# Kernel tuning notes

Hardware: AMD Instinct MI355X
Metric: run time of the kernel (lower is better)

The kernel has to match this reference:

```python
import jax, jax.numpy as jnp
import numpy as np

EMB = 64
HID = 1024
SEQ = 9
BATCH = 4096


def setup_inputs() -> dict:
    key = jax.random.key(0)
    ks = jax.random.split(key, 10)
    s = lambda *sh: 1.0 / np.sqrt(sh[-1])
    return {
        "observed": jax.random.normal(ks[0], (SEQ, BATCH, 2), dtype=jnp.float32),
        "W_emb": jax.random.normal(ks[1], (EMB, 2), dtype=jnp.float32) * s(2),
        "b_emb": jnp.zeros((EMB,), dtype=jnp.float32),
        "W_ih": jax.random.normal(ks[2], (4 * HID, EMB), dtype=jnp.float32) * s(EMB),
        "b_ih": jnp.zeros((4 * HID,), dtype=jnp.float32),
        "W_hh": jax.random.normal(ks[3], (4 * HID, HID), dtype=jnp.float32) * s(HID),
        "b_hh": jnp.zeros((4 * HID,), dtype=jnp.float32),
        "W_out": jax.random.normal(ks[4], (5, HID), dtype=jnp.float32) * s(HID),
        "b_out": jnp.zeros((5,), dtype=jnp.float32),
        "n_predict": 12,
    }


def _cell(x, h, c, W_ih, b_ih, W_hh, b_hh):
    # torch.nn.LSTMCell gate math, gate order i, f, g, o
    gates = x @ W_ih.T + b_ih + h @ W_hh.T + b_hh  # [B, 4H]
    i, f, g, o = jnp.split(gates, 4, axis=-1)
    c_new = jax.nn.sigmoid(f) * c + jax.nn.sigmoid(i) * jnp.tanh(g)
    h_new = jax.nn.sigmoid(o) * jnp.tanh(c_new)
    return h_new, c_new


def reference(observed, W_emb, b_emb, W_ih, b_ih, W_hh, b_hh, W_out, b_out, n_predict):
    B = observed.shape[1]
    H = W_hh.shape[1]
    h0 = jnp.zeros((B, H), dtype=observed.dtype)
    c0 = jnp.zeros((B, H), dtype=observed.dtype)

    diffs = observed[1:] - observed[:-1]  # [SEQ-1, B, 2]

    def obs_step(carry, d):
        h, c = carry
        emb = jax.nn.relu(d @ W_emb.T + b_emb)  # [B, EMB]
        h, c = _cell(emb, h, c, W_ih, b_ih, W_hh, b_hh)
        normal = h @ W_out.T + b_out  # [B, 5]
        return (h, c), normal

    (h, c), normals_obs = jax.lax.scan(obs_step, (h0, c0), diffs)
    new_vel = normals_obs[-1][:, :2]

    def pred_step(carry, _):
        h, c, nv = carry
        emb = jax.nn.relu(jax.lax.stop_gradient(nv) @ W_emb.T + b_emb)
        h, c = _cell(emb, h, c, W_ih, b_ih, W_hh, b_hh)
        normal = h @ W_out.T + b_out
        return (h, c, normal[:, :2]), normal

    (_, _, _), normals_pred = jax.lax.scan(
        pred_step, (h, c, new_vel), None, length=n_predict - 1)

    # training-mode output: stacked raw 'normal' params, shape [SEQ-1+n_predict-1, B, 5]
    return jnp.concatenate([normals_obs, normals_pred], axis=0)
```

## Files before the change

kernel.cpp:

```cpp
#include <hip/hip_runtime.h>
#include <stdint.h>
#include <stddef.h>

#define BATCH 4096
#define HID   1024
#define EMB   64
#define NKH   32
#define NSTEP 19
#define NOBS  8
#define WSL   139264

typedef _Float16 f16;
typedef _Float16 half8 __attribute__((ext_vector_type(8)));
typedef float    float4v __attribute__((ext_vector_type(4)));

__device__ __forceinline__ float sigm(float x) { return 1.f / (1.f + __expf(-x)); }
__device__ __forceinline__ float tanh_f(float x) { return 1.f - 2.f / (__expf(2.f * x) + 1.f); }

__global__ void pack_kernel(const float* __restrict__ W_ih, const float* __restrict__ b_ih,
                            const float* __restrict__ W_hh, const float* __restrict__ b_hh,
                            f16* __restrict__ Wsw, float* __restrict__ bc) {
  int gid = blockIdx.x * blockDim.x + threadIdx.x;
  int tt = gid / WSL;
  int rem = gid - tt * WSL;
  int kt = rem >> 12;
  int ni = (rem >> 9) & 7;
  int lane = (rem >> 3) & 63;
  int e = rem & 7;
  int p = tt * 128 + ni * 16 + (lane & 15);
  int g = (p >> 4) & 3;
  int u = (p >> 8) * 64 + ((p >> 6) & 3) * 16 + (p & 15);
  int orig = g * HID + u;
  int k = kt * 32 + ((lane >> 4) << 3) + e;
  float val = (k < EMB) ? W_ih[orig * EMB + k] : W_hh[orig * HID + (k - EMB)];
  Wsw[gid] = (f16)val;
  if (k == 0) bc[p] = b_ih[orig] + b_hh[orig];
}

__global__ __launch_bounds__(256, 3)
void gemm_cell_kernel(const f16* __restrict__ Xp, const f16* __restrict__ Wsw,
                      const float* __restrict__ bc,
                      f16* __restrict__ c_ws, f16* __restrict__ Xn,
                      float* __restrict__ po_ws, const float* __restrict__ W_out,
                      const float* __restrict__ obs_t, const float* __restrict__ outprev,
                      int mode, const float* __restrict__ W_emb,
                      const float* __restrict__ b_emb) {
  __shared__ float pol[64 * 4 * 5];

  const int tid = threadIdx.x;
  const int lane = tid & 63;
  const int wn = tid >> 6;
  const int l15 = lane & 15;
  const int quad = lane >> 4;
  const int sh = wn >> 1, nq = wn & 1;

  const int id = blockIdx.x;
  const int x = id & 7, rr0 = id >> 3;
  const int bn = x * 2 + (rr0 & 1);
  const int bm = rr0 >> 1;
  const int slice = bn * 2 + sh;

  float4v acc[4][4];
#pragma unroll
  for (int mi = 0; mi < 4; ++mi)
#pragma unroll
    for (int ni = 0; ni < 4; ++ni) acc[mi][ni] = (float4v){0.f, 0.f, 0.f, 0.f};

  const f16* aB = Xp + (size_t)(bm * 4) * (NKH * 512) + lane * 8;
  const f16* bB = Wsw + (size_t)slice * WSL + (size_t)2 * 4096 + (nq * 4) * 512 + lane * 8;

  {
    float d0[4], d1[4];
#pragma unroll
    for (int mi = 0; mi < 4; ++mi) {
      const int row = (bm * 4 + mi) * 16 + l15;
      if (mode <= 1) {
        const float* o = obs_t + (size_t)row * 2;
        d0[mi] = o[BATCH * 2] - o[0];
        d1[mi] = o[BATCH * 2 + 1] - o[1];
      } else {
        d0[mi] = outprev[(size_t)row * 5 + 0];
        d1[mi] = outprev[(size_t)row * 5 + 1];
      }
    }
#pragma unroll
    for (int kt = 0; kt < 2; ++kt) {
      float w0[8], w1[8], be[8];
#pragma unroll
      for (int e = 0; e < 8; ++e) {
        const int j = kt * 32 + quad * 8 + e;
        w0[e] = W_emb[2 * j];
        w1[e] = W_emb[2 * j + 1];
        be[e] = b_emb[j];
      }
      half8 bfe[4];
#pragma unroll
      for (int ni = 0; ni < 4; ++ni)
        bfe[ni] = *(const half8*)(Wsw + (size_t)slice * WSL + kt * 4096 + (nq * 4 + ni) * 512 + lane * 8);
#pragma unroll
      for (int mi = 0; mi < 4; ++mi) {
        half8 ae;
#pragma unroll
        for (int e = 0; e < 8; ++e)
          ae[e] = (f16)fmaxf(d0[mi] * w0[e] + d1[mi] * w1[e] + be[e], 0.f);
#pragma unroll
        for (int ni = 0; ni < 4; ++ni)
          acc[mi][ni] = __builtin_amdgcn_mfma_f32_16x16x32_f16(ae, bfe[ni], acc[mi][ni], 0, 0, 0);
      }
    }
  }

  if (mode != 0) {
    half8 afA[4], bfA[4], afB[4], bfB[4];
#define LOADF(af, bf, kh)                                                      \
  do {                                                                         \
    _Pragma("unroll") for (int mi = 0; mi < 4; ++mi)                           \
        af[mi] = *(const half8*)(aB + mi * (NKH * 512) + (kh) * 512);          \
    _Pragma("unroll") for (int ni = 0; ni < 4; ++ni)                           \
        bf[ni] = *(const half8*)(bB + (size_t)(kh) * 4096 + ni * 512);         \
  } while (0)
#define MFMA_ALL(af, bf)                                                       \
  do {                                                                         \
    __builtin_amdgcn_s_setprio(1);                                             \
    _Pragma("unroll") for (int mi = 0; mi < 4; ++mi)                           \
    _Pragma("unroll") for (int ni = 0; ni < 4; ++ni)                           \
        acc[mi][ni] =                                                          \
            __builtin_amdgcn_mfma_f32_16x16x32_f16(af[mi], bf[ni], acc[mi][ni], 0, 0, 0); \
    __builtin_amdgcn_s_setprio(0);                                             \
  } while (0)
    LOADF(afA, bfA, 0);
    for (int i = 0; i < NKH / 2; ++i) {
      const int k1 = 2 * i + 1;
      LOADF(afB, bfB, k1);
      MFMA_ALL(afA, bfA);
      if (k1 + 1 < NKH) LOADF(afA, bfA, k1 + 1);
      MFMA_ALL(afB, bfB);
    }
#undef LOADF
#undef MFMA_ALL
  }

  float bb[4];
#pragma unroll
  for (int ni = 0; ni < 4; ++ni) bb[ni] = bc[bn * 256 + wn * 64 + ni * 16 + l15];
  const int u = bn * 64 + wn * 16 + l15;
  float wo[5];
#pragma unroll
  for (int o = 0; o < 5; ++o) wo[o] = W_out[o * HID + u];

  f16* cbase = c_ws + ((size_t)(bm * 16 + bn) * 256 + tid) * 16;
  half8 cv[2];
  if (mode != 0) {
#pragma unroll
    for (int q = 0; q < 2; ++q) cv[q] = *(const half8*)(cbase + q * 8);
  }

#pragma unroll
  for (int mi = 0; mi < 4; ++mi) {
#pragma unroll
    for (int r = 0; r < 4; ++r) {
      const int rl = mi * 16 + quad * 4 + r;
      const int row = bm * 64 + rl;
      const int ci = mi * 4 + r;
      float gi = acc[mi][0][r] + bb[0];
      float gf = acc[mi][1][r] + bb[1];
      float gg = acc[mi][2][r] + bb[2];
      float go = acc[mi][3][r] + bb[3];
      float co = (mode == 0) ? 0.f : (float)cv[ci >> 3][ci & 7];
      float cn = sigm(gf) * co + sigm(gi) * tanh_f(gg);
      cv[ci >> 3][ci & 7] = (f16)cn;
      float h = sigm(go) * tanh_f(cn);
      Xn[(((size_t)(row >> 4) * NKH + slice) * 64 + (quad * 4 + r) +
          16 * ((wn & 1) * 2 + (l15 >> 3))) * 8 + (l15 & 7)] = (f16)h;
      float pa[5];
#pragma unroll
      for (int o = 0; o < 5; ++o) pa[o] = h * wo[o];
#pragma unroll
      for (int o = 0; o < 5; ++o) {
        pa[o] += __shfl_xor(pa[o], 1, 64);
        pa[o] += __shfl_xor(pa[o], 2, 64);
        pa[o] += __shfl_xor(pa[o], 4, 64);
        pa[o] += __shfl_xor(pa[o], 8, 64);
      }
      if (l15 == 0) {
#pragma unroll
        for (int o = 0; o < 5; ++o) pol[(rl * 4 + wn) * 5 + o] = pa[o];
      }
    }
  }
#pragma unroll
  for (int q = 0; q < 2; ++q) *(half8*)(cbase + q * 8) = cv[q];

  __syncthreads();
  for (int idx = tid; idx < 320; idx += 256) {
    const int rl = idx / 5, o = idx - rl * 5;
    float s = 0.f;
#pragma unroll
    for (int j = 0; j < 4; ++j) s += pol[(rl * 4 + j) * 5 + o];
    po_ws[((size_t)bn * BATCH + bm * 64 + rl) * 5 + o] = s;
  }
}

__global__ __launch_bounds__(256)
void reduce_kernel(const float* __restrict__ po_ws, const float* __restrict__ b_out,
                   float* __restrict__ out_t) {
  const int tid = threadIdx.x;
  const int r0 = blockIdx.x * 32;
  if (tid < 160) {
    const int rowl = tid / 5, o = tid - rowl * 5;
    const int row = r0 + rowl;
    float s = 0.f;
#pragma unroll
    for (int g = 0; g < 16; ++g) s += po_ws[((size_t)g * BATCH + row) * 5 + o];
    out_t[(size_t)row * 5 + o] = s + b_out[o];
  }
}

extern "C" void kernel_launch(void* const* d_in, const int* in_sizes, int n_in,
                              void* d_out, int out_size, void* d_ws, size_t ws_size,
                              hipStream_t stream) {
  const float* observed = (const float*)d_in[0];
  const float* W_emb = (const float*)d_in[1];
  const float* b_emb = (const float*)d_in[2];
  const float* W_ih = (const float*)d_in[3];
  const float* b_ih = (const float*)d_in[4];
  const float* W_hh = (const float*)d_in[5];
  const float* b_hh = (const float*)d_in[6];
  const float* W_out = (const float*)d_in[7];
  const float* b_out = (const float*)d_in[8];
  float* out = (float*)d_out;

  uint8_t* ws = (uint8_t*)d_ws;
  const size_t WSW_BYTES = (size_t)32 * WSL * sizeof(f16);
  const size_t XH_BYTES = (size_t)256 * NKH * 64 * 8 * sizeof(f16);
  f16* Wsw = (f16*)ws;
  float* bc = (float*)(ws + WSW_BYTES);
  f16* X0 = (f16*)(ws + WSW_BYTES + 16384);
  f16* X1 = (f16*)(ws + WSW_BYTES + 16384 + XH_BYTES);
  f16* c_ws = (f16*)(ws + WSW_BYTES + 16384 + 2 * XH_BYTES);
  float* po_ws = (float*)(ws + WSW_BYTES + 16384 + 2 * XH_BYTES + (size_t)BATCH * HID * 2);

  pack_kernel<<<(32 * WSL) / 256, 256, 0, stream>>>(W_ih, b_ih, W_hh, b_hh, Wsw, bc);

  for (int t = 0; t < NSTEP; ++t) {
    f16* Xc = (t & 1) ? X1 : X0;
    f16* Xq = (t & 1) ? X0 : X1;
    const int mode = (t == 0) ? 0 : (t < NOBS ? 1 : 2);
    gemm_cell_kernel<<<1024, 256, 0, stream>>>(
        Xq, Wsw, bc, c_ws, Xc, po_ws, W_out,
        observed + (size_t)t * BATCH * 2, out + (size_t)(t - 1) * BATCH * 5,
        mode, W_emb, b_emb);
    reduce_kernel<<<BATCH / 32, 256, 0, stream>>>(po_ws, b_out, out + (size_t)t * BATCH * 5);
  }
}
```

Measured before the change: 1.135 ms.

## Move output projection out of GEMM epilogue into separate kernel reading h

The W_out projection, with its shuffle reductions, shared-memory partials and per-slice partial-sum buffer, is removed from the LSTM GEMM epilogue. A new out_kernel reads the fp16 h from the swizzled X buffer and computes the 5 outputs per row with one wave per row. The K loop is also rewritten as a fully unrolled double-buffered loop. This trims epilogue work and register pressure in the main kernel. In exchange it re-reads h from memory and computes the projection from fp16-rounded h instead of fp32 h.

```diff
diff --git a/kernel.cpp b/kernel.cpp
--- a/kernel.cpp
+++ b/kernel.cpp
@@ -41,12 +41,9 @@
 void gemm_cell_kernel(const f16* __restrict__ Xp, const f16* __restrict__ Wsw,
                       const float* __restrict__ bc,
                       f16* __restrict__ c_ws, f16* __restrict__ Xn,
-                      float* __restrict__ po_ws, const float* __restrict__ W_out,
                       const float* __restrict__ obs_t, const float* __restrict__ outprev,
                       int mode, const float* __restrict__ W_emb,
                       const float* __restrict__ b_emb) {
-  __shared__ float pol[64 * 4 * 5];
-
   const int tid = threadIdx.x;
   const int lane = tid & 63;
   const int wn = tid >> 6;
@@ -67,7 +64,7 @@
     for (int ni = 0; ni < 4; ++ni) acc[mi][ni] = (float4v){0.f, 0.f, 0.f, 0.f};
 
   const f16* aB = Xp + (size_t)(bm * 4) * (NKH * 512) + lane * 8;
-  const f16* bB = Wsw + (size_t)slice * WSL + (size_t)2 * 4096 + (nq * 4) * 512 + lane * 8;
+  const f16* bB = Wsw + (size_t)slice * WSL + 2 * 4096 + (nq * 4) * 512 + lane * 8;
 
   {
     float d0[4], d1[4];
@@ -111,42 +108,33 @@
   }
 
   if (mode != 0) {
-    half8 afA[4], bfA[4], afB[4], bfB[4];
-#define LOADF(af, bf, kh)                                                      \
+    half8 af[2][4], bf[2][4];
+#define LOADT(buf, kh)                                                         \
   do {                                                                         \
     _Pragma("unroll") for (int mi = 0; mi < 4; ++mi)                           \
-        af[mi] = *(const half8*)(aB + mi * (NKH * 512) + (kh) * 512);          \
+        af[buf][mi] = *(const half8*)(aB + mi * (NKH * 512) + (kh) * 512);     \
     _Pragma("unroll") for (int ni = 0; ni < 4; ++ni)                           \
-        bf[ni] = *(const half8*)(bB + (size_t)(kh) * 4096 + ni * 512);         \
+        bf[buf][ni] = *(const half8*)(bB + (kh) * 4096 + ni * 512);            \
   } while (0)
-#define MFMA_ALL(af, bf)                                                       \
-  do {                                                                         \
-    __builtin_amdgcn_s_setprio(1);                                             \
-    _Pragma("unroll") for (int mi = 0; mi < 4; ++mi)                           \
-    _Pragma("unroll") for (int ni = 0; ni < 4; ++ni)                           \
-        acc[mi][ni] =                                                          \
-            __builtin_amdgcn_mfma_f32_16x16x32_f16(af[mi], bf[ni], acc[mi][ni], 0, 0, 0); \
-    __builtin_amdgcn_s_setprio(0);                                             \
-  } while (0)
-    LOADF(afA, bfA, 0);
-    for (int i = 0; i < NKH / 2; ++i) {
-      const int k1 = 2 * i + 1;
-      LOADF(afB, bfB, k1);
-      MFMA_ALL(afA, bfA);
-      if (k1 + 1 < NKH) LOADF(afA, bfA, k1 + 1);
-      MFMA_ALL(afB, bfB);
-    }
-#undef LOADF
-#undef MFMA_ALL
+    LOADT(0, 0);
+#pragma unroll
+    for (int kh = 0; kh < NKH; ++kh) {
+      if (kh + 1 < NKH) LOADT((kh + 1) & 1, kh + 1);
+      __builtin_amdgcn_s_setprio(1);
+#pragma unroll
+      for (int mi = 0; mi < 4; ++mi)
+#pragma unroll
+        for (int ni = 0; ni < 4; ++ni)
+          acc[mi][ni] = __builtin_amdgcn_mfma_f32_16x16x32_f16(af[kh & 1][mi], bf[kh & 1][ni],
+                                                               acc[mi][ni], 0, 0, 0);
+      __builtin_amdgcn_s_setprio(0);
+    }
+#undef LOADT
   }
 
   float bb[4];
 #pragma unroll
   for (int ni = 0; ni < 4; ++ni) bb[ni] = bc[bn * 256 + wn * 64 + ni * 16 + l15];
-  const int u = bn * 64 + wn * 16 + l15;
-  float wo[5];
-#pragma unroll
-  for (int o = 0; o < 5; ++o) wo[o] = W_out[o * HID + u];
 
   f16* cbase = c_ws + ((size_t)(bm * 16 + bn) * 256 + tid) * 16;
   half8 cv[2];
@@ -159,8 +147,7 @@
   for (int mi = 0; mi < 4; ++mi) {
 #pragma unroll
     for (int r = 0; r < 4; ++r) {
-      const int rl = mi * 16 + quad * 4 + r;
-      const int row = bm * 64 + rl;
+      const int row = bm * 64 + mi * 16 + quad * 4 + r;
       const int ci = mi * 4 + r;
       float gi = acc[mi][0][r] + bb[0];
       float gf = acc[mi][1][r] + bb[1];
@@ -172,47 +159,48 @@
       float h = sigm(go) * tanh_f(cn);
       Xn[(((size_t)(row >> 4) * NKH + slice) * 64 + (quad * 4 + r) +
           16 * ((wn & 1) * 2 + (l15 >> 3))) * 8 + (l15 & 7)] = (f16)h;
-      float pa[5];
-#pragma unroll
-      for (int o = 0; o < 5; ++o) pa[o] = h * wo[o];
-#pragma unroll
-      for (int o = 0; o < 5; ++o) {
-        pa[o] += __shfl_xor(pa[o], 1, 64);
-        pa[o] += __shfl_xor(pa[o], 2, 64);
-        pa[o] += __shfl_xor(pa[o], 4, 64);
-        pa[o] += __shfl_xor(pa[o], 8, 64);
-      }
-      if (l15 == 0) {
-#pragma unroll
-        for (int o = 0; o < 5; ++o) pol[(rl * 4 + wn) * 5 + o] = pa[o];
-      }
     }
   }
 #pragma unroll
   for (int q = 0; q < 2; ++q) *(half8*)(cbase + q * 8) = cv[q];
-
-  __syncthreads();
-  for (int idx = tid; idx < 320; idx += 256) {
-    const int rl = idx / 5, o = idx - rl * 5;
-    float s = 0.f;
-#pragma unroll
-    for (int j = 0; j < 4; ++j) s += pol[(rl * 4 + j) * 5 + o];
-    po_ws[((size_t)bn * BATCH + bm * 64 + rl) * 5 + o] = s;
-  }
 }
 
 __global__ __launch_bounds__(256)
-void reduce_kernel(const float* __restrict__ po_ws, const float* __restrict__ b_out,
-                   float* __restrict__ out_t) {
+void out_kernel(const f16* __restrict__ Xh, const float* __restrict__ W_out,
+                const float* __restrict__ b_out, float* __restrict__ out_t) {
   const int tid = threadIdx.x;
-  const int r0 = blockIdx.x * 32;
-  if (tid < 160) {
-    const int rowl = tid / 5, o = tid - rowl * 5;
-    const int row = r0 + rowl;
-    float s = 0.f;
-#pragma unroll
-    for (int g = 0; g < 16; ++g) s += po_ws[((size_t)g * BATCH + row) * 5 + o];
-    out_t[(size_t)row * 5 + o] = s + b_out[o];
+  const int lane = tid & 63;
+  const int w = tid >> 6;
+  const int row = blockIdx.x * 4 + w;
+
+  float s[5] = {0.f, 0.f, 0.f, 0.f, 0.f};
+#pragma unroll
+  for (int half = 0; half < 2; ++half) {
+    const int u0 = (lane + half * 64) * 8;
+    const f16* hp = Xh + (((size_t)(row >> 4) * NKH + (u0 >> 5)) * 64 + (row & 15) +
+                          16 * (((u0 >> 4) & 1) * 2 + ((u0 >> 3) & 1))) * 8;
+    half8 hv = *(const half8*)hp;
+#pragma unroll
+    for (int o = 0; o < 5; ++o) {
+      const float* wp = W_out + o * HID + u0;
+      float acc = 0.f;
+#pragma unroll
+      for (int e = 0; e < 8; ++e) acc += (float)hv[e] * wp[e];
+      s[o] += acc;
+    }
+  }
+#pragma unroll
+  for (int o = 0; o < 5; ++o) {
+    s[o] += __shfl_xor(s[o], 1, 64);
+    s[o] += __shfl_xor(s[o], 2, 64);
+    s[o] += __shfl_xor(s[o], 4, 64);
+    s[o] += __shfl_xor(s[o], 8, 64);
+    s[o] += __shfl_xor(s[o], 16, 64);
+    s[o] += __shfl_xor(s[o], 32, 64);
+  }
+  if (lane == 0) {
+#pragma unroll
+    for (int o = 0; o < 5; ++o) out_t[(size_t)row * 5 + o] = s[o] + b_out[o];
   }
 }
 
@@ -238,7 +226,6 @@
   f16* X0 = (f16*)(ws + WSW_BYTES + 16384);
   f16* X1 = (f16*)(ws + WSW_BYTES + 16384 + XH_BYTES);
   f16* c_ws = (f16*)(ws + WSW_BYTES + 16384 + 2 * XH_BYTES);
-  float* po_ws = (float*)(ws + WSW_BYTES + 16384 + 2 * XH_BYTES + (size_t)BATCH * HID * 2);
 
   pack_kernel<<<(32 * WSL) / 256, 256, 0, stream>>>(W_ih, b_ih, W_hh, b_hh, Wsw, bc);
 
@@ -247,9 +234,9 @@
     f16* Xq = (t & 1) ? X0 : X1;
     const int mode = (t == 0) ? 0 : (t < NOBS ? 1 : 2);
     gemm_cell_kernel<<<1024, 256, 0, stream>>>(
-        Xq, Wsw, bc, c_ws, Xc, po_ws, W_out,
+        Xq, Wsw, bc, c_ws, Xc,
         observed + (size_t)t * BATCH * 2, out + (size_t)(t - 1) * BATCH * 5,
         mode, W_emb, b_emb);
-    reduce_kernel<<<BATCH / 32, 256, 0, stream>>>(po_ws, b_out, out + (size_t)t * BATCH * 5);
-  }
-}
+    out_kernel<<<BATCH / 4, 256, 0, stream>>>(Xc, W_out, b_out, out + (size_t)t * BATCH * 5);
+  }
+}
```

Result: no change. 1.124 ms (-0.9%).
